# Kernel tuning notes

Measured on AMD Instinct MI355X. Metric: run time of the kernel, lower is better.

## Reference

```python
import jax, jax.numpy as jnp
import numpy as np

EPS = 1e-5


def conv3x3(x, w, b):
    # x [B,C,H,W], w [O,C,3,3], stride 1, pad 1
    y = jax.lax.conv_general_dilated(x, w, (1, 1), ((1, 1), (1, 1)),
                                     dimension_numbers=('NCHW', 'OIHW', 'NCHW'))
    return y + b[None, :, None, None]


def bilinear_gather(x, py, px):
    # x [B,C,H,W]; sampling locations py,px [B,K,H,W] -> [B,C,K,H,W]
    # Zero padding outside the image (matches deform_conv CUDA semantics:
    # out-of-bound corner values contribute 0).
    B, C, H, W = x.shape
    K = py.shape[1]
    x_flat = x.reshape(B, C, H * W)
    y0 = jnp.floor(py)
    x0 = jnp.floor(px)
    out = jnp.zeros((B, C, K, H, W), x.dtype)
    for dy in (0.0, 1.0):
        for dx in (0.0, 1.0):
            yi = y0 + dy
            xi = x0 + dx
            wgt = (1.0 - jnp.abs(py - yi)) * (1.0 - jnp.abs(px - xi))  # [B,K,H,W]
            valid = (yi >= 0) & (yi <= H - 1) & (xi >= 0) & (xi <= W - 1)
            idx = (jnp.clip(yi, 0, H - 1).astype(jnp.int32) * W
                   + jnp.clip(xi, 0, W - 1).astype(jnp.int32)).reshape(B, -1)
            vals = jax.vmap(lambda xf, i: xf[:, i])(x_flat, idx)  # [B,C,K*H*W]
            out = out + (wgt * valid)[:, None] * vals.reshape(B, C, K, H, W)
    return out


def setup_inputs() -> dict:
    key = jax.random.key(0)
    k1, k2, k3 = jax.random.split(key, 3)
    B, C, O, H, W = 4, 64, 64, 128, 128
    x = jax.random.normal(k1, (B, C, H, W), jnp.float32)
    # offset predictor: small init so predicted offsets are modest (realistic)
    off_w = 0.01 * jax.random.normal(k2, (18, C, 3, 3), jnp.float32)
    off_b = jnp.zeros((18,), jnp.float32)
    dc_w = jax.random.normal(k3, (O, C, 3, 3), jnp.float32) / np.sqrt(C * 9)
    dc_b = jnp.zeros((O,), jnp.float32)
    gamma = jnp.ones((O,), jnp.float32)
    beta = jnp.zeros((O,), jnp.float32)
    return {"x": x, "off_w": off_w, "off_b": off_b, "dc_w": dc_w,
            "dc_b": dc_b, "gamma": gamma, "beta": beta}


def reference(x, off_w, off_b, dc_w, dc_b, gamma, beta):
    B, C, H, W = x.shape
    O = dc_w.shape[0]
    K = 9  # 3x3 kernel
    offset = conv3x3(x, off_w, off_b)              # [B,18,H,W]
    off = offset.reshape(B, K, 2, H, W)            # (dy,dx) per kernel tap, row-major
    dyo, dxo = off[:, :, 0], off[:, :, 1]          # [B,K,H,W]
    k = (jnp.arange(3) - 1).astype(x.dtype)        # kernel taps {-1,0,1}
    kgy = jnp.repeat(k, 3)                         # [9] row-major y offsets
    kgx = jnp.tile(k, 3)                           # [9] row-major x offsets
    hh = jnp.arange(H, dtype=x.dtype)
    ww = jnp.arange(W, dtype=x.dtype)
    # stride 1, pad 1: base point = out_pos - 1 + tap; pad is folded into kgy/kgx
    py = hh[None, None, :, None] + kgy[None, :, None, None] + dyo
    px = ww[None, None, None, :] + kgx[None, :, None, None] + dxo
    sampled = bilinear_gather(x, py, px)           # [B,C,K,H,W]
    y = jnp.einsum('ock,bckhw->bohw', dc_w.reshape(O, C, K), sampled)
    y = y + dc_b[None, :, None, None]
    # BatchNorm2d (training mode: biased batch statistics)
    mu = y.mean(axis=(0, 2, 3), keepdims=True)
    var = y.var(axis=(0, 2, 3), keepdims=True)
    yn = (y - mu) * jax.lax.rsqrt(var + EPS)
    return jax.nn.relu(yn * gamma[None, :, None, None] + beta[None, :, None, None])
```

## Files before the change

### kernel.cpp

```cpp
#include <hip/hip_runtime.h>

#define HH 128
#define WW 128
#define HWSZ (HH * WW)
#define CC 64
#define OO 64
#define BB 4
#define NOFF 18
#define KK 576

#define WS_BG     0
#define WS_BGO    18432
#define WS_SUMS   27648
#define WS_SUMSQ  27712
#define WS_YBUF   27776

typedef __attribute__((ext_vector_type(8))) short short8;
typedef __attribute__((ext_vector_type(4))) int int4v;
typedef __attribute__((ext_vector_type(4))) float f32x4;

__device__ inline unsigned bf16rne(float f) {
  unsigned u = __float_as_uint(f);
  u += 0x7fff + ((u >> 16) & 1);
  return u >> 16;
}

__global__ __launch_bounds__(256) void prep_kernel(
    const float* __restrict__ x, const float* __restrict__ off_w,
    const float* __restrict__ dc_w, unsigned int* __restrict__ xTu,
    int* __restrict__ Bg, int* __restrict__ Bgo, float* __restrict__ sums) {
  int bid = blockIdx.x;
  if (bid < BB * HH) {
    __shared__ float T[CC][WW + 1];
    int b = bid >> 7, h = bid & 127;
    int tw = threadIdx.x & 127, th = threadIdx.x >> 7;
    const float* xp = x + (size_t)b * CC * HWSZ + h * WW;
#pragma unroll 8
    for (int i = 0; i < 32; ++i) {
      int c = i * 2 + th;
      T[c][tw] = xp[c * HWSZ + tw];
    }
    __syncthreads();
    int c2 = threadIdx.x & 31, wq = threadIdx.x >> 5;
    unsigned int* op = xTu + ((size_t)(b * HH + h) * WW) * 32;
#pragma unroll 8
    for (int i = 0; i < 16; ++i) {
      int w = i * 8 + wq;
      unsigned pk = bf16rne(T[2 * c2][w]) | (bf16rne(T[2 * c2 + 1][w]) << 16);
      op[w * 32 + c2] = pk;
    }
  } else {
    int pb = bid - BB * HH;
    int tid = pb * 256 + threadIdx.x;
    int stride = 64 * 256;
    for (int i = tid; i < 72 * 64 * 4; i += stride) {
      int j = i & 3, o = (i >> 2) & 63, g = i >> 8;
      int k2 = g * 4 + j, t = k2 >> 5, jj = k2 & 31;
      unsigned lo = bf16rne(dc_w[o * KK + (2 * jj) * 9 + t]);
      unsigned hi = bf16rne(dc_w[o * KK + (2 * jj + 1) * 9 + t]);
      Bg[i] = (int)(lo | (hi << 16));
    }
    for (int i = tid; i < 72 * 32 * 4; i += stride) {
      int j = i & 3, o = (i >> 2) & 31, g = i >> 7;
      int k2 = g * 4 + j, t = k2 >> 5, jj = k2 & 31;
      unsigned pk = 0;
      if (o < NOFF) {
        unsigned lo = bf16rne(off_w[o * KK + (2 * jj) * 9 + t]);
        unsigned hi = bf16rne(off_w[o * KK + (2 * jj + 1) * 9 + t]);
        pk = lo | (hi << 16);
      }
      Bgo[i] = (int)pk;
    }
    if (tid < 128) sums[tid] = 0.0f;
  }
}

#define G_ISSUE(i, TAP, TL, PH)                                               \
  int4v m##i, da##i, db##i, dc##i, dd##i;                                     \
  {                                                                           \
    int pxl_ = (PH) * 8 + p8;                                                 \
    m##i = *(const int4v*)&Mw[(pxl_ * 9 + (TAP)) * 4];                        \
    unsigned x_ = (unsigned)m##i.x, y_ = (unsigned)m##i.y;                    \
    da##i = *(const int4v*)&xbu[(x_ & 0xffffu) * 32 + cq4];                   \
    db##i = *(const int4v*)&xbu[(x_ >> 16) * 32 + cq4];                       \
    dc##i = *(const int4v*)&xbu[(y_ & 0xffffu) * 32 + cq4];                   \
    dd##i = *(const int4v*)&xbu[(y_ >> 16) * 32 + cq4];                       \
  }

#define G_BLEND(i, TL, PH)                                                    \
  {                                                                           \
    int pxl_ = (PH) * 8 + p8;                                                 \
    float w00_ = __uint_as_float(((unsigned)m##i.z) << 16);                   \
    float w01_ = __uint_as_float(((unsigned)m##i.z) & 0xffff0000u);           \
    float w10_ = __uint_as_float(((unsigned)m##i.w) << 16);                   \
    float w11_ = __uint_as_float(((unsigned)m##i.w) & 0xffff0000u);           \
    int4v pk_;                                                                \
    _Pragma("unroll")                                                         \
    for (int j = 0; j < 4; ++j) {                                             \
      float slo_ = w00_ * __uint_as_float(((unsigned)da##i[j]) << 16);        \
      slo_ = fmaf(w01_, __uint_as_float(((unsigned)db##i[j]) << 16), slo_);   \
      slo_ = fmaf(w10_, __uint_as_float(((unsigned)dc##i[j]) << 16), slo_);   \
      slo_ = fmaf(w11_, __uint_as_float(((unsigned)dd##i[j]) << 16), slo_);   \
      float shi_ = w00_ * __uint_as_float(((unsigned)da##i[j]) & 0xffff0000u);\
      shi_ = fmaf(w01_, __uint_as_float(((unsigned)db##i[j]) & 0xffff0000u), shi_);\
      shi_ = fmaf(w10_, __uint_as_float(((unsigned)dc##i[j]) & 0xffff0000u), shi_);\
      shi_ = fmaf(w11_, __uint_as_float(((unsigned)dd##i[j]) & 0xffff0000u), shi_);\
      pk_[j] = (int)__builtin_amdgcn_perm(__float_as_uint(shi_) + 0x8000u,    \
                                          __float_as_uint(slo_) + 0x8000u,    \
                                          0x07060302u);                       \
    }                                                                         \
    *(int4v*)&A[(p0 + pxl_) * 100 + (TL) * 32 + cq4] = pk_;                   \
  }

__global__ __launch_bounds__(256, 4) void fused_kernel(
    const unsigned int* __restrict__ xTu, const int* __restrict__ Bg,
    const int* __restrict__ Bgo, const float* __restrict__ off_b,
    const float* __restrict__ dc_b, float* __restrict__ ybuf,
    float* __restrict__ sums, float* __restrict__ sumsq) {
  __shared__ __align__(16) int A[4 * 16 * 100];
  __shared__ __align__(16) int M[4 * 144 * 4];
  __shared__ float offL[4][NOFF][16];

  int cg = threadIdx.x >> 6, lane = threadIdx.x & 63;
  int b = blockIdx.x >> 8, rem = blockIdx.x & 255;
  int h = rem >> 1, w0 = (rem & 1) * 64;
  int hw0 = h * WW + w0;
  int p0 = cg * 16;
  int n16 = lane & 15, q = lane >> 4;
  int pg = lane >> 3, part = lane & 7;
  const unsigned int* xbu = xTu + (size_t)b * HWSZ * 32;

  f32x4 acc2[2] = {f32x4{0, 0, 0, 0}, f32x4{0, 0, 0, 0}};
#pragma unroll 1
  for (int chunk = 0; chunk < 3; ++chunk) {
    int cy = h + chunk - 1;
    bool vy = (cy >= 0) && (cy < HH);
    int cys = min(max(cy, 0), HH - 1);
#pragma unroll
    for (int tl = 0; tl < 3; ++tl) {
#pragma unroll
      for (int i = 0; i < 2; ++i) {
        int px = i * 8 + pg;
        int cx = w0 + p0 + px + tl - 1;
        bool v = vy && (cx >= 0) && (cx < WW);
        int cxs = min(max(cx, 0), WW - 1);
        int4v val = *(const int4v*)&xbu[(cys * WW + cxs) * 32 + part * 4];
        if (!v) { val.x = 0; val.y = 0; val.z = 0; val.w = 0; }
        *(int4v*)&A[(p0 + px) * 100 + tl * 32 + part * 4] = val;
      }
    }
#pragma unroll 2
    for (int kk = 0; kk < 6; ++kk) {
      int4v av = *(const int4v*)&A[(p0 + n16) * 100 + kk * 16 + q * 4];
      short8 af = __builtin_bit_cast(short8, av);
      int g = chunk * 24 + kk * 4 + q;
#pragma unroll
      for (int nt = 0; nt < 2; ++nt) {
        int4v bv = *(const int4v*)&Bgo[(g * 32 + nt * 16 + n16) * 4];
        short8 bfr = __builtin_bit_cast(short8, bv);
        acc2[nt] = __builtin_amdgcn_mfma_f32_16x16x32_bf16(af, bfr, acc2[nt], 0, 0, 0);
      }
    }
  }
#pragma unroll
  for (int nt = 0; nt < 2; ++nt) {
    int o = nt * 16 + n16;
    if (o < NOFF) {
      float bv = off_b[o];
#pragma unroll
      for (int r = 0; r < 4; ++r) offL[cg][o][q * 4 + r] = acc2[nt][r] + bv;
    }
  }

  int* Mw = M + cg * 144 * 4;
#pragma unroll
  for (int it = 0; it < 3; ++it) {
    int m = it * 64 + lane;
    if (m < 144) {
      int pxl = (unsigned)m / 9u;
      int t = m - pxl * 9;
      float dy = offL[cg][2 * t][pxl];
      float dx = offL[cg][2 * t + 1][pxl];
      float py = (float)(h + t / 3 - 1) + dy;
      float pxf = (float)(w0 + p0 + pxl + (t % 3) - 1) + dx;
      float fy0 = floorf(py), fx0 = floorf(pxf);
      float ay = py - fy0, ax = pxf - fx0;
      int iy0 = (int)fy0, ix0 = (int)fx0;
      int iy1 = iy0 + 1, ix1 = ix0 + 1;
      float wy0 = 1.0f - ay, wy1 = ay, wx0 = 1.0f - ax, wx1 = ax;
      if (!(iy0 >= 0 && iy0 < HH)) wy0 = 0.0f;
      if (!(iy1 >= 0 && iy1 < HH)) wy1 = 0.0f;
      if (!(ix0 >= 0 && ix0 < WW)) wx0 = 0.0f;
      if (!(ix1 >= 0 && ix1 < WW)) wx1 = 0.0f;
      int cy0 = min(max(iy0, 0), HH - 1), cy1 = min(max(iy1, 0), HH - 1);
      int cx0 = min(max(ix0, 0), WW - 1), cx1 = min(max(ix1, 0), WW - 1);
      int4v mv;
      mv.x = (cy0 * WW + cx0) | ((cy0 * WW + cx1) << 16);
      mv.y = (cy1 * WW + cx0) | ((cy1 * WW + cx1) << 16);
      mv.z = (int)(bf16rne(wy0 * wx0) | (bf16rne(wy0 * wx1) << 16));
      mv.w = (int)(bf16rne(wy1 * wx0) | (bf16rne(wy1 * wx1) << 16));
      *(int4v*)&Mw[m * 4] = mv;
    }
  }

  int p8 = lane >> 3;
  int cq4 = (lane & 7) * 4;
  f32x4 acc[4] = {f32x4{0,0,0,0}, f32x4{0,0,0,0}, f32x4{0,0,0,0}, f32x4{0,0,0,0}};
#pragma unroll 1
  for (int chunk = 0; chunk < 3; ++chunk) {
    int tap0 = chunk * 3;
    G_ISSUE(0, tap0 + 0, 0, 0)
    G_ISSUE(1, tap0 + 0, 0, 1)
    G_ISSUE(2, tap0 + 1, 1, 0)
    G_BLEND(0, 0, 0)
    G_ISSUE(3, tap0 + 1, 1, 1)
    G_BLEND(1, 0, 1)
    G_ISSUE(4, tap0 + 2, 2, 0)
    G_BLEND(2, 1, 0)
    G_ISSUE(5, tap0 + 2, 2, 1)
    G_BLEND(3, 1, 1)
    G_BLEND(4, 2, 0)
    G_BLEND(5, 2, 1)
#pragma unroll 2
    for (int kk = 0; kk < 6; ++kk) {
      int4v av = *(const int4v*)&A[(p0 + n16) * 100 + kk * 16 + q * 4];
      short8 af = __builtin_bit_cast(short8, av);
      int g = chunk * 24 + kk * 4 + q;
#pragma unroll
      for (int nt = 0; nt < 4; ++nt) {
        int4v bv = *(const int4v*)&Bg[(g * 64 + nt * 16 + n16) * 4];
        short8 bfr = __builtin_bit_cast(short8, bv);
        acc[nt] = __builtin_amdgcn_mfma_f32_16x16x32_bf16(af, bfr, acc[nt], 0, 0, 0);
      }
    }
  }

  float* SW = (float*)&A[cg * 1600];
#pragma unroll
  for (int nt = 0; nt < 4; ++nt) {
    int o = nt * 16 + n16;
    float bv = dc_b[o];
    f32x4 r;
    float s = 0.0f, ss = 0.0f;
#pragma unroll
    for (int r0 = 0; r0 < 4; ++r0) {
      r[r0] = acc[nt][r0] + bv;
      s += r[r0];
      ss += r[r0] * r[r0];
    }
    *(f32x4*)(ybuf + (size_t)(b * OO + o) * HWSZ + hw0 + p0 + q * 4) = r;
    s += __shfl_xor(s, 16);  s += __shfl_xor(s, 32);
    ss += __shfl_xor(ss, 16); ss += __shfl_xor(ss, 32);
    if (lane < 16) {
      SW[nt * 16 + lane] = s;
      SW[64 + nt * 16 + lane] = ss;
    }
  }
  __syncthreads();
  if (threadIdx.x < 64) {
    float ts = 0.0f, tq = 0.0f;
#pragma unroll
    for (int wv = 0; wv < 4; ++wv) {
      const float* Sv = (const float*)&A[wv * 1600];
      ts += Sv[threadIdx.x];
      tq += Sv[64 + threadIdx.x];
    }
    atomicAdd(&sums[threadIdx.x], ts);
    atomicAdd(&sumsq[threadIdx.x], tq);
  }
}

__global__ __launch_bounds__(256) void norm_kernel(
    const float* __restrict__ ybuf, const float* __restrict__ sums,
    const float* __restrict__ sumsq, const float* __restrict__ gamma,
    const float* __restrict__ beta, float* __restrict__ out) {
  int gid = blockIdx.x * 256 + threadIdx.x;
  int flat = gid << 2;
  int o = (flat >> 14) & 63;
  const float invN = 1.0f / (float)(BB * HWSZ);
  float mean = sums[o] * invN;
  float var = sumsq[o] * invN - mean * mean;
  float rstd = rsqrtf(var + 1e-5f);
  float g = gamma[o] * rstd;
  float bta = beta[o] - mean * g;
  float4 v = ((const float4*)ybuf)[gid];
  float4 r;
  r.x = fmaxf(v.x * g + bta, 0.0f);
  r.y = fmaxf(v.y * g + bta, 0.0f);
  r.z = fmaxf(v.z * g + bta, 0.0f);
  r.w = fmaxf(v.w * g + bta, 0.0f);
  ((float4*)out)[gid] = r;
}

extern "C" void kernel_launch(void* const* d_in, const int* in_sizes, int n_in,
                              void* d_out, int out_size, void* d_ws, size_t ws_size,
                              hipStream_t stream) {
  const float* x     = (const float*)d_in[0];
  const float* off_w = (const float*)d_in[1];
  const float* off_b = (const float*)d_in[2];
  const float* dc_w  = (const float*)d_in[3];
  const float* dc_b  = (const float*)d_in[4];
  const float* gamma = (const float*)d_in[5];
  const float* beta  = (const float*)d_in[6];
  float* ws = (float*)d_ws;
  int*   Bg     = (int*)(ws + WS_BG);
  int*   Bgo    = (int*)(ws + WS_BGO);
  float* sums   = ws + WS_SUMS;
  float* sumsq  = ws + WS_SUMSQ;
  float* ybuf   = ws + WS_YBUF;
  float* out = (float*)d_out;
  unsigned int* xTu = (unsigned int*)d_out;

  prep_kernel<<<BB * HH + 64, 256, 0, stream>>>(x, off_w, dc_w, xTu, Bg, Bgo, sums);
  fused_kernel<<<BB * HWSZ / 64, 256, 0, stream>>>(xTu, Bg, Bgo, off_b, dc_b, ybuf, sums, sumsq);
  norm_kernel<<<BB * OO * HWSZ / (4 * 256), 256, 0, stream>>>(ybuf, sums, sumsq, gamma, beta, out);
}
```

Before: 142.6 us.

## Fully unroll tap chunks and prefetch next chunk's gathers across MFMA phases

Replaces the three-iteration chunk loop with a fully unrolled sequence in which gather loads for the next chunk's taps are issued before the current chunk's MFMA phase. Scheduling barriers pin the issue/blend interleaving so the compiler cannot reorder it. The goal is to hide global gather latency behind blending and matrix math. In exchange, more gather data stays live in registers, which adds pressure under the 256x4 launch bound and may cause spills.

After: 149.4 us. 1.05x slower.

```diff
diff --git a/kernel.cpp b/kernel.cpp
--- a/kernel.cpp
+++ b/kernel.cpp
@@ -75,16 +75,17 @@
   }
 }
 
-#define G_ISSUE(i, TAP, TL, PH)                                               \
-  int4v m##i, da##i, db##i, dc##i, dd##i;                                     \
+#define SB __builtin_amdgcn_sched_barrier(0);
+
+#define G_ISSUE(i, TAP, PH)                                                   \
+  int4v m##i, da##i, db##i, dcv##i, dd##i;                                    \
   {                                                                           \
-    int pxl_ = (PH) * 8 + p8;                                                 \
-    m##i = *(const int4v*)&Mw[(pxl_ * 9 + (TAP)) * 4];                        \
+    m##i = *(const int4v*)&Mw[(((PH) * 8 + p8) * 9 + (TAP)) * 4];             \
     unsigned x_ = (unsigned)m##i.x, y_ = (unsigned)m##i.y;                    \
-    da##i = *(const int4v*)&xbu[(x_ & 0xffffu) * 32 + cq4];                   \
-    db##i = *(const int4v*)&xbu[(x_ >> 16) * 32 + cq4];                       \
-    dc##i = *(const int4v*)&xbu[(y_ & 0xffffu) * 32 + cq4];                   \
-    dd##i = *(const int4v*)&xbu[(y_ >> 16) * 32 + cq4];                       \
+    da##i  = *(const int4v*)&xbu[(x_ & 0xffffu) * 32 + cq4];                  \
+    db##i  = *(const int4v*)&xbu[(x_ >> 16) * 32 + cq4];                      \
+    dcv##i = *(const int4v*)&xbu[(y_ & 0xffffu) * 32 + cq4];                  \
+    dd##i  = *(const int4v*)&xbu[(y_ >> 16) * 32 + cq4];                      \
   }
 
 #define G_BLEND(i, TL, PH)                                                    \
@@ -99,17 +100,33 @@
     for (int j = 0; j < 4; ++j) {                                             \
       float slo_ = w00_ * __uint_as_float(((unsigned)da##i[j]) << 16);        \
       slo_ = fmaf(w01_, __uint_as_float(((unsigned)db##i[j]) << 16), slo_);   \
-      slo_ = fmaf(w10_, __uint_as_float(((unsigned)dc##i[j]) << 16), slo_);   \
+      slo_ = fmaf(w10_, __uint_as_float(((unsigned)dcv##i[j]) << 16), slo_);  \
       slo_ = fmaf(w11_, __uint_as_float(((unsigned)dd##i[j]) << 16), slo_);   \
       float shi_ = w00_ * __uint_as_float(((unsigned)da##i[j]) & 0xffff0000u);\
       shi_ = fmaf(w01_, __uint_as_float(((unsigned)db##i[j]) & 0xffff0000u), shi_);\
-      shi_ = fmaf(w10_, __uint_as_float(((unsigned)dc##i[j]) & 0xffff0000u), shi_);\
+      shi_ = fmaf(w10_, __uint_as_float(((unsigned)dcv##i[j]) & 0xffff0000u), shi_);\
       shi_ = fmaf(w11_, __uint_as_float(((unsigned)dd##i[j]) & 0xffff0000u), shi_);\
       pk_[j] = (int)__builtin_amdgcn_perm(__float_as_uint(shi_) + 0x8000u,    \
                                           __float_as_uint(slo_) + 0x8000u,    \
                                           0x07060302u);                       \
     }                                                                         \
     *(int4v*)&A[(p0 + pxl_) * 100 + (TL) * 32 + cq4] = pk_;                   \
+  }
+
+#define MFMA_CHUNK(CH)                                                        \
+  {                                                                           \
+    _Pragma("unroll 2")                                                       \
+    for (int kk = 0; kk < 6; ++kk) {                                          \
+      int4v av = *(const int4v*)&A[(p0 + n16) * 100 + kk * 16 + q * 4];       \
+      short8 af = __builtin_bit_cast(short8, av);                             \
+      int g = (CH) * 24 + kk * 4 + q;                                         \
+      _Pragma("unroll")                                                       \
+      for (int nt = 0; nt < 4; ++nt) {                                        \
+        int4v bv = *(const int4v*)&Bg[(g * 64 + nt * 16 + n16) * 4];          \
+        short8 bfr = __builtin_bit_cast(short8, bv);                          \
+        acc[nt] = __builtin_amdgcn_mfma_f32_16x16x32_bf16(af, bfr, acc[nt], 0, 0, 0); \
+      }                                                                       \
+    }                                                                         \
   }
 
 __global__ __launch_bounds__(256, 4) void fused_kernel(
@@ -206,34 +223,28 @@
   int p8 = lane >> 3;
   int cq4 = (lane & 7) * 4;
   f32x4 acc[4] = {f32x4{0,0,0,0}, f32x4{0,0,0,0}, f32x4{0,0,0,0}, f32x4{0,0,0,0}};
-#pragma unroll 1
-  for (int chunk = 0; chunk < 3; ++chunk) {
-    int tap0 = chunk * 3;
-    G_ISSUE(0, tap0 + 0, 0, 0)
-    G_ISSUE(1, tap0 + 0, 0, 1)
-    G_ISSUE(2, tap0 + 1, 1, 0)
-    G_BLEND(0, 0, 0)
-    G_ISSUE(3, tap0 + 1, 1, 1)
-    G_BLEND(1, 0, 1)
-    G_ISSUE(4, tap0 + 2, 2, 0)
-    G_BLEND(2, 1, 0)
-    G_ISSUE(5, tap0 + 2, 2, 1)
-    G_BLEND(3, 1, 1)
-    G_BLEND(4, 2, 0)
-    G_BLEND(5, 2, 1)
-#pragma unroll 2
-    for (int kk = 0; kk < 6; ++kk) {
-      int4v av = *(const int4v*)&A[(p0 + n16) * 100 + kk * 16 + q * 4];
-      short8 af = __builtin_bit_cast(short8, av);
-      int g = chunk * 24 + kk * 4 + q;
-#pragma unroll
-      for (int nt = 0; nt < 4; ++nt) {
-        int4v bv = *(const int4v*)&Bg[(g * 64 + nt * 16 + n16) * 4];
-        short8 bfr = __builtin_bit_cast(short8, bv);
-        acc[nt] = __builtin_amdgcn_mfma_f32_16x16x32_bf16(af, bfr, acc[nt], 0, 0, 0);
-      }
-    }
-  }
+  G_ISSUE(0, 0, 0) G_ISSUE(1, 0, 1) G_ISSUE(2, 1, 0) G_ISSUE(3, 1, 1) SB
+  G_BLEND(0, 0, 0)  G_ISSUE(4, 2, 0)  SB
+  G_BLEND(1, 0, 1)  G_ISSUE(5, 2, 1)  SB
+  G_BLEND(2, 1, 0)  G_ISSUE(6, 3, 0)  SB
+  G_BLEND(3, 1, 1)  G_ISSUE(7, 3, 1)  SB
+  G_BLEND(4, 2, 0)  G_ISSUE(8, 4, 0)  SB
+  G_BLEND(5, 2, 1)  G_ISSUE(9, 4, 1)  SB
+  MFMA_CHUNK(0) SB
+  G_BLEND(6, 0, 0)  G_ISSUE(10, 5, 0) SB
+  G_BLEND(7, 0, 1)  G_ISSUE(11, 5, 1) SB
+  G_BLEND(8, 1, 0)  G_ISSUE(12, 6, 0) SB
+  G_BLEND(9, 1, 1)  G_ISSUE(13, 6, 1) SB
+  G_BLEND(10, 2, 0) G_ISSUE(14, 7, 0) SB
+  G_BLEND(11, 2, 1) G_ISSUE(15, 7, 1) SB
+  MFMA_CHUNK(1) SB
+  G_BLEND(12, 0, 0) G_ISSUE(16, 8, 0) SB
+  G_BLEND(13, 0, 1) G_ISSUE(17, 8, 1) SB
+  G_BLEND(14, 1, 0) SB
+  G_BLEND(15, 1, 1) SB
+  G_BLEND(16, 2, 0) SB
+  G_BLEND(17, 2, 1) SB
+  MFMA_CHUNK(2)
 
   float* SW = (float*)&A[cg * 1600];
 #pragma unroll
```
